# Kernel tuning notes

Measured on AMD Instinct MI355X. Metric: run time of the kernel, lower is better.

The kernel has to match this reference:

```python
import jax, jax.numpy as jnp
import numpy as np

EMB = 768
HEADS = 12
DEPTH = EMB // HEADS
B, L = 8, 1024


def setup_inputs() -> dict:
    key = jax.random.key(0)
    ks = jax.random.split(key, 11)
    s = 1.0 / np.sqrt(EMB)
    inp = {
        "v": jax.random.normal(ks[0], (B, L, EMB), jnp.float32),
        "k": jax.random.normal(ks[1], (B, L, EMB), jnp.float32),
        "q": jax.random.normal(ks[2], (B, L, EMB), jnp.float32),
        # torch Linear weights: [out_features, in_features]
        "wq_w": jax.random.normal(ks[3], (EMB, EMB), jnp.float32) * s,
        "wq_b": jax.random.normal(ks[4], (EMB,), jnp.float32) * s,
        "wk_w": jax.random.normal(ks[5], (EMB, EMB), jnp.float32) * s,
        "wk_b": jax.random.normal(ks[6], (EMB,), jnp.float32) * s,
        "wv_w": jax.random.normal(ks[7], (EMB, EMB), jnp.float32) * s,
        "wv_b": jax.random.normal(ks[8], (EMB,), jnp.float32) * s,
        "dense_w": jax.random.normal(ks[9], (EMB, EMB), jnp.float32) * s,
        "dense_b": jax.random.normal(ks[10], (EMB,), jnp.float32) * s,
    }
    return inp


def _split_heads(x):
    b, l, _ = x.shape
    return x.reshape(b, l, HEADS, DEPTH).transpose(0, 2, 1, 3)  # [b,h,l,d]


def reference(v, k, q, wq_w, wq_b, wk_w, wk_b, wv_w, wv_b, dense_w, dense_b):
    qh = _split_heads(q @ wq_w.T + wq_b)
    kh = _split_heads(k @ wk_w.T + wk_b)
    vh = _split_heads(v @ wv_w.T + wv_b)
    # NOTE: module scales by sqrt(embedding_dim), not sqrt(depth)
    scale = 1.0 / jnp.sqrt(jnp.asarray(EMB, qh.dtype))
    score = jnp.einsum("bhqd,bhkd->bhqk", qh, kh) * scale
    attn_w = jax.nn.softmax(score, axis=-1)  # [b,h,lq,lk]
    logits = jnp.einsum("bhqk,bhkd->bhqd", attn_w, vh)
    concat = logits.transpose(0, 2, 1, 3).reshape(q.shape[0], -1, EMB)
    attention = concat @ dense_w.T + dense_b  # dropout p=0 -> identity
    return attention, attn_w
```

## Files before the change

kernel.cpp:

```cpp
#include <hip/hip_runtime.h>

#define EMB 768
#define NH 12
#define HD 64
#define BBATCH 8
#define LL 1024
#define BL (BBATCH * LL)

typedef __attribute__((ext_vector_type(8))) short bf16x8;
typedef __attribute__((ext_vector_type(4))) float f32x4;

__device__ __forceinline__ unsigned int f2bfu(float f) {
  unsigned int u = __builtin_bit_cast(unsigned int, f);
  return (u + 0x7FFFu + ((u >> 16) & 1u)) >> 16;
}

__device__ __forceinline__ f32x4 mfma16(bf16x8 a, bf16x8 b, f32x4 c) {
  return __builtin_amdgcn_mfma_f32_16x16x32_bf16(a, b, c, 0, 0, 0);
}

__global__ __launch_bounds__(256) void convert_w_kernel(
    const float* __restrict__ wq, const float* __restrict__ wk,
    const float* __restrict__ wv, const float* __restrict__ wd,
    unsigned short* __restrict__ out) {
  const int n = EMB * EMB;
  int e = (blockIdx.x * 256 + threadIdx.x) * 4;
  int which = e / n;
  int off = e - which * n;
  const float* src = (which == 0) ? wq : (which == 1) ? wk : (which == 2) ? wv : wd;
  float4 v4 = *reinterpret_cast<const float4*>(src + off);
  uint2 o;
  o.x = f2bfu(v4.x) | (f2bfu(v4.y) << 16);
  o.y = f2bfu(v4.z) | (f2bfu(v4.w) << 16);
  *reinterpret_cast<uint2*>(out + e) = o;
}

template <int MODE>
__global__ __launch_bounds__(256) void gemm_xwt_kernel(
    const void* __restrict__ Xv, const unsigned short* __restrict__ W,
    const float* __restrict__ bias, void* __restrict__ outp, float out_scale) {
  constexpr bool IN_F32 = (MODE != 2);
  extern __shared__ char smem[];
  unsigned short* Ab = reinterpret_cast<unsigned short*>(smem);
  unsigned short* Bb = Ab + 128 * 32;

  const int t = threadIdx.x;
  const int lane = t & 63, wid = t >> 6;
  const int wr = wid >> 1, wc = wid & 1;
  const int lrow = lane & 15, lgrp = lane >> 4;
  const int bm0 = blockIdx.x * 128, bn0 = blockIdx.y * 128;

  f32x4 acc[4][4];
#pragma unroll
  for (int i = 0; i < 4; ++i)
#pragma unroll
    for (int j = 0; j < 4; ++j) acc[i][j] = (f32x4){0.f, 0.f, 0.f, 0.f};

  float4 aF[2][2];
  uint4 aB[2];
  uint4 bB[2];

  const int ar = t >> 2, as = t & 3;
  const int rb = t >> 1, sb = (t & 1) * 2;

  auto load_regs = [&](int kt) {
    const int k0 = kt * 32;
    if constexpr (IN_F32) {
      const float* X = reinterpret_cast<const float*>(Xv);
      const float* g0 = X + (size_t)(bm0 + ar) * EMB + k0 + as * 8;
      aF[0][0] = reinterpret_cast<const float4*>(g0)[0];
      aF[0][1] = reinterpret_cast<const float4*>(g0)[1];
      const float* g1 = g0 + (size_t)64 * EMB;
      aF[1][0] = reinterpret_cast<const float4*>(g1)[0];
      aF[1][1] = reinterpret_cast<const float4*>(g1)[1];
    } else {
      const unsigned short* X = reinterpret_cast<const unsigned short*>(Xv);
      const uint4* g = reinterpret_cast<const uint4*>(X + (size_t)(bm0 + rb) * EMB + k0 + sb * 8);
      aB[0] = g[0];
      aB[1] = g[1];
    }
    const uint4* gw = reinterpret_cast<const uint4*>(W + (size_t)(bn0 + rb) * EMB + k0 + sb * 8);
    bB[0] = gw[0];
    bB[1] = gw[1];
  };

  auto write_lds = [&]() {
    if constexpr (IN_F32) {
#pragma unroll
      for (int it = 0; it < 2; ++it) {
        int r = ar + it * 64;
        uint4 pk;
        pk.x = f2bfu(aF[it][0].x) | (f2bfu(aF[it][0].y) << 16);
        pk.y = f2bfu(aF[it][0].z) | (f2bfu(aF[it][0].w) << 16);
        pk.z = f2bfu(aF[it][1].x) | (f2bfu(aF[it][1].y) << 16);
        pk.w = f2bfu(aF[it][1].z) | (f2bfu(aF[it][1].w) << 16);
        *reinterpret_cast<uint4*>(Ab + r * 32 + ((as ^ (r & 3)) * 8)) = pk;
      }
    } else {
      *reinterpret_cast<uint4*>(Ab + rb * 32 + ((sb ^ (rb & 3)) * 8)) = aB[0];
      *reinterpret_cast<uint4*>(Ab + rb * 32 + (((sb + 1) ^ (rb & 3)) * 8)) = aB[1];
    }
    *reinterpret_cast<uint4*>(Bb + rb * 32 + ((sb ^ (rb & 3)) * 8)) = bB[0];
    *reinterpret_cast<uint4*>(Bb + rb * 32 + (((sb + 1) ^ (rb & 3)) * 8)) = bB[1];
  };

  auto compute = [&]() {
    bf16x8 a[4], b[4];
    const int sw = (lgrp ^ (lrow & 3)) * 8;
#pragma unroll
    for (int i = 0; i < 4; ++i) {
      int r = wr * 64 + i * 16 + lrow;
      a[i] = *reinterpret_cast<const bf16x8*>(Ab + r * 32 + sw);
      int c = wc * 64 + i * 16 + lrow;
      b[i] = *reinterpret_cast<const bf16x8*>(Bb + c * 32 + sw);
    }
#pragma unroll
    for (int i = 0; i < 4; ++i)
#pragma unroll
      for (int j = 0; j < 4; ++j) acc[i][j] = mfma16(a[i], b[j], acc[i][j]);
  };

  load_regs(0);
  write_lds();
  __syncthreads();
#pragma unroll 1
  for (int kt = 0; kt < 24; ++kt) {
    if (kt < 23) load_regs(kt + 1);
    compute();
    __syncthreads();
    if (kt < 23) {
      write_lds();
      __syncthreads();
    }
  }

  if constexpr (MODE == 0) {
    unsigned short* out = reinterpret_cast<unsigned short*>(outp);
#pragma unroll
    for (int jj = 0; jj < 4; ++jj) {
      int C = bn0 + wc * 64 + jj * 16 + lrow;
      float bv = bias[C];
      int hh = C >> 6, dd = C & 63;
#pragma unroll
      for (int i = 0; i < 4; ++i)
#pragma unroll
        for (int j2 = 0; j2 < 4; ++j2) {
          int R = bm0 + wr * 64 + i * 16 + lgrp * 4 + j2;
          int bidx = R >> 10, l = R & 1023;
          out[(((size_t)(bidx * NH + hh) * 1024 + l) << 6) + dd] =
              (unsigned short)f2bfu((acc[i][jj][j2] + bv) * out_scale);
        }
    }
  }

  if constexpr (MODE == 1) {
    __syncthreads();
    unsigned short* T = reinterpret_cast<unsigned short*>(smem);
#pragma unroll
    for (int jj = 0; jj < 4; ++jj) {
      int cl = wc * 64 + jj * 16 + lrow;
      float bv = bias[bn0 + cl];
#pragma unroll
      for (int i = 0; i < 4; ++i)
#pragma unroll
        for (int j2 = 0; j2 < 4; ++j2) {
          int rl = wr * 64 + i * 16 + lgrp * 4 + j2;
          T[cl * 136 + rl] = (unsigned short)f2bfu(acc[i][jj][j2] + bv);
        }
    }
    __syncthreads();
    unsigned short* out = reinterpret_cast<unsigned short*>(outp);
    int cl = t >> 1, rh = (t & 1) * 64;
    int C = bn0 + cl, hh = C >> 6, dd = C & 63;
    int Rg = bm0 + rh, bidx = Rg >> 10, l0 = Rg & 1023;
    size_t obase = ((size_t)(bidx * NH + hh) * 64 + dd) * 1024 + l0;
#pragma unroll
    for (int q8 = 0; q8 < 8; ++q8) {
      uint4 val = *reinterpret_cast<const uint4*>(T + cl * 136 + rh + q8 * 8);
      *reinterpret_cast<uint4*>(out + obase + q8 * 8) = val;
    }
  }

  if constexpr (MODE == 2) {
    float* out = reinterpret_cast<float*>(outp);
#pragma unroll
    for (int jj = 0; jj < 4; ++jj) {
      int C = bn0 + wc * 64 + jj * 16 + lrow;
      float bv = bias[C];
#pragma unroll
      for (int i = 0; i < 4; ++i)
#pragma unroll
        for (int j2 = 0; j2 < 4; ++j2) {
          int R = bm0 + wr * 64 + i * 16 + lgrp * 4 + j2;
          out[(size_t)R * EMB + C] = acc[i][jj][j2] + bv;
        }
    }
  }
}

__global__ __launch_bounds__(256) void attn_kernel(
    const unsigned short* __restrict__ qh, const unsigned short* __restrict__ kh,
    const unsigned short* __restrict__ vhT, float* __restrict__ attn_w,
    unsigned short* __restrict__ concat) {
  __shared__ unsigned short Pl[16 * 1024];
  __shared__ float red[2][4][16];

  const int t = threadIdx.x;
  const int lane = t & 63, w = t >> 6;
  const int lrow = lane & 15, lgrp = lane >> 4;
  const int qt = blockIdx.x, pair = blockIdx.y;
  const int b = pair / NH, h = pair - b * NH;
  const int q0 = qt * 16;
  const unsigned short* qbase = qh + (size_t)pair * (LL * HD);
  const unsigned short* kbase = kh + (size_t)pair * (LL * HD);
  const unsigned short* vbase = vhT + (size_t)pair * (HD * LL);

  bf16x8 aq[2];
#pragma unroll
  for (int c = 0; c < 2; ++c)
    aq[c] = *reinterpret_cast<const bf16x8*>(qbase + (size_t)(q0 + lrow) * HD + c * 32 + lgrp * 8);

  f32x4 acc[16];
#pragma unroll
  for (int f = 0; f < 16; ++f) acc[f] = (f32x4){0.f, 0.f, 0.f, 0.f};

  const int k0 = w * 256;
#pragma unroll
  for (int f = 0; f < 16; ++f) {
    const unsigned short* kr = kbase + (size_t)(k0 + f * 16 + lrow) * HD + lgrp * 8;
    bf16x8 b0 = *reinterpret_cast<const bf16x8*>(kr);
    bf16x8 b1 = *reinterpret_cast<const bf16x8*>(kr + 32);
    acc[f] = mfma16(aq[0], b0, acc[f]);
    acc[f] = mfma16(aq[1], b1, acc[f]);
  }

  float m0[4], s0[4];
#pragma unroll
  for (int j = 0; j < 4; ++j) m0[j] = acc[0][j];
#pragma unroll
  for (int f = 1; f < 16; ++f)
#pragma unroll
    for (int j = 0; j < 4; ++j) m0[j] = fmaxf(m0[j], acc[f][j]);
#pragma unroll
  for (int mask = 1; mask < 16; mask <<= 1)
#pragma unroll
    for (int j = 0; j < 4; ++j) m0[j] = fmaxf(m0[j], __shfl_xor(m0[j], mask));
  if ((lane & 15) == 0) {
#pragma unroll
    for (int j = 0; j < 4; ++j) red[0][w][lgrp * 4 + j] = m0[j];
  }
  __syncthreads();
  float M[4];
#pragma unroll
  for (int j = 0; j < 4; ++j) {
    int r = lgrp * 4 + j;
    M[j] = fmaxf(fmaxf(red[0][0][r], red[0][1][r]), fmaxf(red[0][2][r], red[0][3][r]));
    s0[j] = 0.f;
  }
#pragma unroll
  for (int f = 0; f < 16; ++f)
#pragma unroll
    for (int j = 0; j < 4; ++j) {
      float p = __expf(acc[f][j] - M[j]);
      acc[f][j] = p;
      s0[j] += p;
    }
#pragma unroll
  for (int mask = 1; mask < 16; mask <<= 1)
#pragma unroll
    for (int j = 0; j < 4; ++j) s0[j] += __shfl_xor(s0[j], mask);
  if ((lane & 15) == 0) {
#pragma unroll
    for (int j = 0; j < 4; ++j) red[1][w][lgrp * 4 + j] = s0[j];
  }
  __syncthreads();
  float inv[4];
#pragma unroll
  for (int j = 0; j < 4; ++j) {
    int r = lgrp * 4 + j;
    inv[j] = 1.0f / (red[1][0][r] + red[1][1][r] + red[1][2][r] + red[1][3][r]);
  }

  float* awp = attn_w + (size_t)pair * (LL * LL);
#pragma unroll
  for (int f = 0; f < 16; ++f) {
    int col = k0 + f * 16 + lrow;
#pragma unroll
    for (int j = 0; j < 4; ++j) {
      int prow = lgrp * 4 + j;
      float v = acc[f][j] * inv[j];
      __builtin_nontemporal_store(v, awp + (size_t)(q0 + prow) * LL + col);
      int byte = (prow * 2048 + col * 2) ^ ((prow & 7) << 4);
      *reinterpret_cast<unsigned short*>(reinterpret_cast<char*>(Pl) + byte) =
          (unsigned short)f2bfu(v);
    }
  }
  __syncthreads();

  f32x4 o = (f32x4){0.f, 0.f, 0.f, 0.f};
  const unsigned short* vrow = vbase + (size_t)(w * 16 + lrow) * LL;
#pragma unroll
  for (int kk = 0; kk < 32; ++kk) {
    int byte = (lrow * 2048 + (kk * 32 + lgrp * 8) * 2) ^ ((lrow & 7) << 4);
    bf16x8 pa = *reinterpret_cast<const bf16x8*>(reinterpret_cast<char*>(Pl) + byte);
    bf16x8 vb = *reinterpret_cast<const bf16x8*>(vrow + kk * 32 + lgrp * 8);
    o = mfma16(pa, vb, o);
  }
#pragma unroll
  for (int j = 0; j < 4; ++j) {
    int row = q0 + lgrp * 4 + j;
    int cc = h * 64 + w * 16 + lrow;
    concat[((size_t)b * LL + row) * EMB + cc] = (unsigned short)f2bfu(o[j]);
  }
}

extern "C" void kernel_launch(void* const* d_in, const int* in_sizes, int n_in,
                              void* d_out, int out_size, void* d_ws, size_t ws_size,
                              hipStream_t stream) {
  const float* v = (const float*)d_in[0];
  const float* k = (const float*)d_in[1];
  const float* q = (const float*)d_in[2];
  const float* wq_w = (const float*)d_in[3];
  const float* wq_b = (const float*)d_in[4];
  const float* wk_w = (const float*)d_in[5];
  const float* wk_b = (const float*)d_in[6];
  const float* wv_w = (const float*)d_in[7];
  const float* wv_b = (const float*)d_in[8];
  const float* dw = (const float*)d_in[9];
  const float* db = (const float*)d_in[10];

  float* out_attn = (float*)d_out;
  float* out_w = out_attn + (size_t)BL * EMB;

  if (ws_size < 55050240u) return;
  unsigned short* ws = (unsigned short*)d_ws;
  unsigned short* wqb16 = ws;
  unsigned short* wkb16 = wqb16 + EMB * EMB;
  unsigned short* wvb16 = wkb16 + EMB * EMB;
  unsigned short* wdb16 = wvb16 + EMB * EMB;
  unsigned short* qhb = wdb16 + EMB * EMB;
  unsigned short* khb = qhb + (size_t)BL * EMB;
  unsigned short* vtb = khb + (size_t)BL * EMB;
  unsigned short* cat = vtb + (size_t)BL * EMB;

  convert_w_kernel<<<dim3(2304), dim3(256), 0, stream>>>(wq_w, wk_w, wv_w, dw, ws);

  const float scale = 0.036084391824351615f;
  dim3 gg(64, 6);
  gemm_xwt_kernel<0><<<gg, 256, 16384, stream>>>(q, wqb16, wq_b, qhb, scale);
  gemm_xwt_kernel<0><<<gg, 256, 16384, stream>>>(k, wkb16, wk_b, khb, 1.0f);
  gemm_xwt_kernel<1><<<gg, 256, 128 * 136 * 2, stream>>>(v, wvb16, wv_b, vtb, 1.0f);

  attn_kernel<<<dim3(64, 96), 256, 0, stream>>>(qhb, khb, vtb, out_w, cat);

  gemm_xwt_kernel<2><<<gg, 256, 16384, stream>>>(cat, wdb16, db, out_attn, 1.0f);
}
```

Before: 390.9 us.

## Transpose QK^T MFMA output so each lane owns one query row and vectorize stores

The MFMA operands for the score product are swapped, so each lane holds four consecutive key columns of a single query row. Row max and sum reductions then need only two cross-lane shuffles instead of four per element group, and the attention-weight writes become 16-byte nontemporal vector stores. The bf16 probabilities are written to LDS as packed 8-byte chunks. The change also prefetches the first eight V fragments before the softmax and raises wave priority around the MFMA loops, at the cost of extra registers for the prefetch.

Result: slower. 400.8 us (+2.5%).

```diff
diff --git a/kernel.cpp b/kernel.cpp
--- a/kernel.cpp
+++ b/kernel.cpp
@@ -225,87 +225,76 @@
   for (int f = 0; f < 16; ++f) acc[f] = (f32x4){0.f, 0.f, 0.f, 0.f};
 
   const int k0 = w * 256;
+  __builtin_amdgcn_s_setprio(1);
 #pragma unroll
   for (int f = 0; f < 16; ++f) {
     const unsigned short* kr = kbase + (size_t)(k0 + f * 16 + lrow) * HD + lgrp * 8;
     bf16x8 b0 = *reinterpret_cast<const bf16x8*>(kr);
     bf16x8 b1 = *reinterpret_cast<const bf16x8*>(kr + 32);
-    acc[f] = mfma16(aq[0], b0, acc[f]);
-    acc[f] = mfma16(aq[1], b1, acc[f]);
-  }
-
-  float m0[4], s0[4];
-#pragma unroll
-  for (int j = 0; j < 4; ++j) m0[j] = acc[0][j];
-#pragma unroll
-  for (int f = 1; f < 16; ++f)
-#pragma unroll
-    for (int j = 0; j < 4; ++j) m0[j] = fmaxf(m0[j], acc[f][j]);
-#pragma unroll
-  for (int mask = 1; mask < 16; mask <<= 1)
-#pragma unroll
-    for (int j = 0; j < 4; ++j) m0[j] = fmaxf(m0[j], __shfl_xor(m0[j], mask));
-  if ((lane & 15) == 0) {
-#pragma unroll
-    for (int j = 0; j < 4; ++j) red[0][w][lgrp * 4 + j] = m0[j];
-  }
+    acc[f] = mfma16(b0, aq[0], acc[f]);
+    acc[f] = mfma16(b1, aq[1], acc[f]);
+  }
+  __builtin_amdgcn_s_setprio(0);
+
+  const unsigned short* vrow = vbase + (size_t)(w * 16 + lrow) * LL;
+  bf16x8 vpre[8];
+#pragma unroll
+  for (int kk = 0; kk < 8; ++kk)
+    vpre[kk] = *reinterpret_cast<const bf16x8*>(vrow + kk * 32 + lgrp * 8);
+
+  float m = acc[0][0];
+#pragma unroll
+  for (int f = 0; f < 16; ++f)
+#pragma unroll
+    for (int j = 0; j < 4; ++j) m = fmaxf(m, acc[f][j]);
+  m = fmaxf(m, __shfl_xor(m, 16));
+  m = fmaxf(m, __shfl_xor(m, 32));
+  if (lane < 16) red[0][w][lane] = m;
   __syncthreads();
-  float M[4];
-#pragma unroll
-  for (int j = 0; j < 4; ++j) {
-    int r = lgrp * 4 + j;
-    M[j] = fmaxf(fmaxf(red[0][0][r], red[0][1][r]), fmaxf(red[0][2][r], red[0][3][r]));
-    s0[j] = 0.f;
-  }
+  float M = fmaxf(fmaxf(red[0][0][lrow], red[0][1][lrow]),
+                  fmaxf(red[0][2][lrow], red[0][3][lrow]));
+  float s = 0.f;
 #pragma unroll
   for (int f = 0; f < 16; ++f)
 #pragma unroll
     for (int j = 0; j < 4; ++j) {
-      float p = __expf(acc[f][j] - M[j]);
+      float p = __expf(acc[f][j] - M);
       acc[f][j] = p;
-      s0[j] += p;
-    }
-#pragma unroll
-  for (int mask = 1; mask < 16; mask <<= 1)
-#pragma unroll
-    for (int j = 0; j < 4; ++j) s0[j] += __shfl_xor(s0[j], mask);
-  if ((lane & 15) == 0) {
-#pragma unroll
-    for (int j = 0; j < 4; ++j) red[1][w][lgrp * 4 + j] = s0[j];
-  }
+      s += p;
+    }
+  s += __shfl_xor(s, 16);
+  s += __shfl_xor(s, 32);
+  if (lane < 16) red[1][w][lane] = s;
   __syncthreads();
-  float inv[4];
-#pragma unroll
-  for (int j = 0; j < 4; ++j) {
-    int r = lgrp * 4 + j;
-    inv[j] = 1.0f / (red[1][0][r] + red[1][1][r] + red[1][2][r] + red[1][3][r]);
-  }
-
-  float* awp = attn_w + (size_t)pair * (LL * LL);
+  float inv = 1.0f / (red[1][0][lrow] + red[1][1][lrow] + red[1][2][lrow] + red[1][3][lrow]);
+
+  float* awp = attn_w + (size_t)pair * (LL * LL) + (size_t)(q0 + lrow) * LL + k0 + lgrp * 4;
+  char* Plb = reinterpret_cast<char*>(Pl);
 #pragma unroll
   for (int f = 0; f < 16; ++f) {
-    int col = k0 + f * 16 + lrow;
-#pragma unroll
-    for (int j = 0; j < 4; ++j) {
-      int prow = lgrp * 4 + j;
-      float v = acc[f][j] * inv[j];
-      __builtin_nontemporal_store(v, awp + (size_t)(q0 + prow) * LL + col);
-      int byte = (prow * 2048 + col * 2) ^ ((prow & 7) << 4);
-      *reinterpret_cast<unsigned short*>(reinterpret_cast<char*>(Pl) + byte) =
-          (unsigned short)f2bfu(v);
-    }
+    float p0 = acc[f][0] * inv, p1 = acc[f][1] * inv;
+    float p2 = acc[f][2] * inv, p3 = acc[f][3] * inv;
+    f32x4 o = {p0, p1, p2, p3};
+    __builtin_nontemporal_store(o, reinterpret_cast<f32x4*>(awp + f * 16));
+    uint2 pb;
+    pb.x = f2bfu(p0) | (f2bfu(p1) << 16);
+    pb.y = f2bfu(p2) | (f2bfu(p3) << 16);
+    int byte = (lrow * 2048 + (k0 + f * 16 + lgrp * 4) * 2) ^ ((lrow & 7) << 4);
+    *reinterpret_cast<uint2*>(Plb + byte) = pb;
   }
   __syncthreads();
 
   f32x4 o = (f32x4){0.f, 0.f, 0.f, 0.f};
-  const unsigned short* vrow = vbase + (size_t)(w * 16 + lrow) * LL;
+  __builtin_amdgcn_s_setprio(1);
 #pragma unroll
   for (int kk = 0; kk < 32; ++kk) {
     int byte = (lrow * 2048 + (kk * 32 + lgrp * 8) * 2) ^ ((lrow & 7) << 4);
-    bf16x8 pa = *reinterpret_cast<const bf16x8*>(reinterpret_cast<char*>(Pl) + byte);
-    bf16x8 vb = *reinterpret_cast<const bf16x8*>(vrow + kk * 32 + lgrp * 8);
+    bf16x8 pa = *reinterpret_cast<const bf16x8*>(Plb + byte);
+    bf16x8 vb = (kk < 8) ? vpre[kk]
+                         : *reinterpret_cast<const bf16x8*>(vrow + kk * 32 + lgrp * 8);
     o = mfma16(pa, vb, o);
   }
+  __builtin_amdgcn_s_setprio(0);
 #pragma unroll
   for (int j = 0; j < 4; ++j) {
     int row = q0 + lgrp * 4 + j;
@@ -351,7 +340,7 @@
   gemm_xwt_kernel<0><<<gg, 256, 16384, stream>>>(k, wkb16, wk_b, khb, 1.0f);
   gemm_xwt_kernel<1><<<gg, 256, 128 * 136 * 2, stream>>>(v, wvb16, wv_b, vtb, 1.0f);
 
-  attn_kernel<<<dim3(64, 96), 256, 0, stream>>>(qhb, khb, vtb, out_w, cat);
+  attn_kernel<<<dim3(64, 96), dim3(256), 0, stream>>>(qhb, khb, vtb, out_w, cat);
 
   gemm_xwt_kernel<2><<<gg, 256, 16384, stream>>>(cat, wdb16, db, out_attn, 1.0f);
 }
```
